# Kernel tuning notes

Measured on AMD Instinct MI355X. Metric: run time of the kernel, lower is better.

Reference implementation:

```python
import jax, jax.numpy as jnp
import numpy as np

B, S, H = 1, 2048, 2048
I = 1408            # moe intermediate size
E = 16              # n_routed_experts
K = 6               # num_experts_per_tok
G = 4               # n_group
KG = 2              # topk_group
NSH = 2             # n_shared_experts -> shared intermediate = NSH*I
RSF = 2.5           # routed_scaling_factor
CAP = 2 * (B * S * K) // E


def setup_inputs() -> dict:
    key = jax.random.key(0)
    ks = jax.random.split(key, 9)
    sh = NSH * I
    s_h = 1.0 / np.sqrt(H).astype(np.float32)
    s_i = 1.0 / np.sqrt(I).astype(np.float32)
    s_s = 1.0 / np.sqrt(sh).astype(np.float32)
    return {
        "x": jax.random.normal(ks[0], (B, S, H), jnp.float32),
        "gate_w": jax.random.normal(ks[1], (E, H), jnp.float32) * s_h,
        "gate_bias": jnp.zeros((E,), jnp.float32),
        "w_gate": jax.random.normal(ks[2], (E, H, I), jnp.float32) * s_h,
        "w_up": jax.random.normal(ks[3], (E, H, I), jnp.float32) * s_h,
        "w_down": jax.random.normal(ks[4], (E, I, H), jnp.float32) * s_i,
        "ws_gate": jax.random.normal(ks[5], (H, sh), jnp.float32) * s_h,
        "ws_up": jax.random.normal(ks[6], (H, sh), jnp.float32) * s_h,
        "ws_down": jax.random.normal(ks[7], (sh, H), jnp.float32) * s_s,
    }


def _gate(x2d, gate_w, gate_bias):
    # MoEGate: fp32 linear -> sigmoid -> noaux_tc group-limited top-k
    logits = x2d.astype(jnp.float32) @ gate_w.astype(jnp.float32).T     # [T,E]
    scores = jax.nn.sigmoid(logits)
    scores_c = scores + gate_bias                                       # e_score_correction_bias
    T = scores.shape[0]
    gs = scores_c.reshape(T, G, E // G)
    top2, _ = jax.lax.top_k(gs, 2)
    group_scores = top2.sum(-1)                                         # [T,G] sum of top-2 per group
    _, gidx = jax.lax.top_k(group_scores, KG)                           # keep top KG groups
    gmask = jnp.zeros((T, G), scores.dtype).at[jnp.arange(T)[:, None], gidx].set(1.0)
    smask = jnp.repeat(gmask, E // G, axis=1)                           # [T,E]
    tmp = jnp.where(smask > 0, scores_c, 0.0)
    _, topk_idx = jax.lax.top_k(tmp, K)                                 # [T,K]
    topk_w = jnp.take_along_axis(scores, topk_idx, axis=1)              # weights from UNbiased scores
    topk_w = topk_w / (topk_w.sum(-1, keepdims=True) + 1e-20)           # norm_topk_prob
    topk_w = topk_w * RSF
    return topk_idx, topk_w


def reference(x, gate_w, gate_bias, w_gate, w_up, w_down, ws_gate, ws_up, ws_down):
    T = B * S
    x2d = x.reshape(T, H)
    topk_idx, topk_w = _gate(x2d, gate_w, gate_bias)

    # ---- dispatch: sort (token,k) assignments by expert id (grouped-GEMM layout) ----
    flat_e = topk_idx.reshape(-1)                       # [T*K]
    order = jnp.argsort(flat_e, stable=True)
    sorted_e = flat_e[order]
    counts = jnp.bincount(flat_e, length=E)             # batch_sizes per expert
    starts = jnp.concatenate([jnp.zeros((1,), counts.dtype), jnp.cumsum(counts)[:-1]])
    pos = jnp.arange(T * K) - starts[sorted_e]          # slot within expert bucket
    tok = order // K                                    # source token of each assignment
    buf = jnp.zeros((E, CAP, H), x.dtype).at[sorted_e, pos].set(x2d[tok], mode="drop")

    # ---- grouped SwiGLU expert FFN (gmm equivalent) ----
    g = jnp.einsum("ech,ehi->eci", buf, w_gate)
    u = jnp.einsum("ech,ehi->eci", buf, w_up)
    y_e = jnp.einsum("eci,eih->ech", jax.nn.silu(g) * u, w_down)

    # ---- combine: gather back, weight, scatter-add per token ----
    keep = (pos < CAP).astype(x.dtype)
    y_sorted = y_e[sorted_e, jnp.minimum(pos, CAP - 1)] * keep[:, None]
    w_flat = topk_w.reshape(-1)[order]
    y = jnp.zeros((T, H), x.dtype).at[tok].add(y_sorted * w_flat[:, None])

    # ---- shared experts (dense SwiGLU on all tokens) ----
    sg = x2d @ ws_gate
    su = x2d @ ws_up
    y = y + (jax.nn.silu(sg) * su) @ ws_down
    return y.reshape(B, S, H)
```

## Files before the change

### kernel.cpp

```cpp
#include <hip/hip_runtime.h>

typedef unsigned short u16;
typedef u16  u16x8 __attribute__((ext_vector_type(8)));
typedef u16  u16x4 __attribute__((ext_vector_type(4)));
typedef short s16x8 __attribute__((ext_vector_type(8)));
typedef float f32x4 __attribute__((ext_vector_type(4)));

static constexpr int TT   = 2048;
static constexpr int HD   = 2048;
static constexpr int ID   = 1408;
static constexpr int NE   = 16;
static constexpr int TOPK = 6;
static constexpr int CAPE = 1536;
static constexpr int SHD  = 2816;
static constexpr float RSF_ = 2.5f;
static constexpr int PGRID = 1024;

__device__ __forceinline__ u16 f2b(float f) {
  unsigned int u = __builtin_bit_cast(unsigned int, f);
  unsigned int r = (u + 0x7FFFu + ((u >> 16) & 1u)) >> 16;
  return (u16)r;
}
__device__ __forceinline__ float b2f(u16 u) {
  unsigned int v = ((unsigned int)u) << 16;
  return __builtin_bit_cast(float, v);
}

__device__ __forceinline__ void gl_lds16(const u16* gp, u16* lp) {
  __builtin_amdgcn_global_load_lds(
      (const __attribute__((address_space(1))) void*)(unsigned long long)(const void*)gp,
      (__attribute__((address_space(3))) void*)(unsigned int)(unsigned long long)(void*)lp,
      16, 0, 0);
}

__device__ __forceinline__ void seq_map(int idx, int mtiles, int ntiles,
                                        int& bx, int& by, int& e) {
  bx = idx % mtiles;
  int tq = idx / mtiles;
  by = tq % ntiles;
  e  = tq / ntiles;
}

__global__ __launch_bounds__(256) void k_cvt(const float* __restrict__ in, u16* __restrict__ out) {
  size_t i = (size_t)blockIdx.x * 256 + threadIdx.x;
  const float4* p = (const float4*)in;
  float4 v0 = p[i * 2], v1 = p[i * 2 + 1];
  u16x8 o = { f2b(v0.x), f2b(v0.y), f2b(v0.z), f2b(v0.w),
              f2b(v1.x), f2b(v1.y), f2b(v1.z), f2b(v1.w) };
  *(u16x8*)(out + i * 8) = o;
}

__global__ __launch_bounds__(64) void k_init(int* c) {
  if (threadIdx.x < 16) c[threadIdx.x] = 0;
}

__global__ __launch_bounds__(256) void k_gate2(const float* __restrict__ x,
    const float* __restrict__ gw, const float* __restrict__ gb,
    int* __restrict__ topk_idx, float* __restrict__ topk_w) {
  const int t = threadIdx.x;
  const int tok0 = blockIdx.x * 8;
  const int i  = t >> 5;
  const int sub = t & 31;
  const int e  = sub & 15;
  const int kh = sub >> 4;
  const float4* xr = (const float4*)(x + (size_t)(tok0 + i) * HD) + kh * (HD / 8);
  const float4* wr = (const float4*)(gw + (size_t)e * HD) + kh * (HD / 8);
  float acc = 0.f;
  #pragma unroll 8
  for (int k = 0; k < HD / 8; ++k) {
    float4 a = xr[k], b = wr[k];
    acc += a.x * b.x + a.y * b.y;
    acc += a.z * b.z + a.w * b.w;
  }
  acc += __shfl_down(acc, 16);
  __shared__ float lg[8][16];
  if (sub < 16) lg[i][e] = acc;
  __syncthreads();
  if (t >= 8) return;
  const int tok = tok0 + t;
  float s[NE], sc[NE];
  #pragma unroll
  for (int ee = 0; ee < NE; ++ee) {
    s[ee]  = 1.f / (1.f + expf(-lg[t][ee]));
    sc[ee] = s[ee] + gb[ee];
  }
  float gs[4];
  #pragma unroll
  for (int g = 0; g < 4; ++g) {
    float m1 = -1e30f, m2 = -1e30f;
    #pragma unroll
    for (int j = 0; j < 4; ++j) {
      float v = sc[g * 4 + j];
      if (v > m1) { m2 = m1; m1 = v; } else if (v > m2) m2 = v;
    }
    gs[g] = m1 + m2;
  }
  int g0 = 0;
  #pragma unroll
  for (int g = 1; g < 4; ++g) if (gs[g] > gs[g0]) g0 = g;
  int g1 = -1; float g1v = -1e30f;
  #pragma unroll
  for (int g = 0; g < 4; ++g) {
    if (g == g0) continue;
    if (g1 < 0 || gs[g] > g1v) { g1 = g; g1v = gs[g]; }
  }
  float tmp[NE];
  #pragma unroll
  for (int ee = 0; ee < NE; ++ee) {
    int g = ee >> 2;
    tmp[ee] = (g == g0 || g == g1) ? sc[ee] : 0.0f;
  }
  unsigned used = 0;
  float wsum = 0.f;
  int idxs[TOPK]; float wv[TOPK];
  #pragma unroll
  for (int k = 0; k < TOPK; ++k) {
    int best = -1; float bv = -2e30f;
    #pragma unroll
    for (int ee = 0; ee < NE; ++ee) {
      bool ok = (((used >> ee) & 1u) == 0u) && (tmp[ee] > bv);
      if (ok) { bv = tmp[ee]; best = ee; }
    }
    used |= 1u << best;
    float sv = 0.f;
    #pragma unroll
    for (int ee = 0; ee < NE; ++ee) if (ee == best) sv = s[ee];
    idxs[k] = best; wv[k] = sv; wsum += sv;
  }
  float scale = RSF_ / (wsum + 1e-20f);
  #pragma unroll
  for (int k = 0; k < TOPK; ++k) {
    topk_idx[tok * TOPK + k] = idxs[k];
    topk_w[tok * TOPK + k]   = wv[k] * scale;
  }
}

__global__ __launch_bounds__(256) void k_count_pos(const int* __restrict__ topk_idx,
    int* __restrict__ rowidx, int* __restrict__ tok_of_row, int* __restrict__ counts) {
  const int e = blockIdx.x, t = threadIdx.x;
  __shared__ int pref[256];
  const int t0 = t * 8;
  int c = 0;
  for (int tt = t0; tt < t0 + 8; ++tt)
    for (int k = 0; k < TOPK; ++k) c += (topk_idx[tt * TOPK + k] == e) ? 1 : 0;
  pref[t] = c;
  __syncthreads();
  for (int off = 1; off < 256; off <<= 1) {
    int v = (t >= off) ? pref[t - off] : 0;
    __syncthreads();
    pref[t] += v;
    __syncthreads();
  }
  int run = pref[t] - c;
  if (t == 255) counts[e] = (pref[255] < CAPE) ? pref[255] : CAPE;
  for (int tt = t0; tt < t0 + 8; ++tt)
    for (int k = 0; k < TOPK; ++k)
      if (topk_idx[tt * TOPK + k] == e) {
        if (run < CAPE) {
          rowidx[tt * TOPK + k] = e * CAPE + run;
          tok_of_row[e * CAPE + run] = tt;
        } else {
          rowidx[tt * TOPK + k] = -1;
        }
        ++run;
      }
}

__global__ __launch_bounds__(256) void k_transpose_cvt(const float* __restrict__ in,
    u16* __restrict__ out, int R, int Cc, long zin, long zout) {
  __shared__ float tile[64][65];
  const float* src = in + (size_t)blockIdx.z * zin;
  u16* dst = out + (size_t)blockIdx.z * zout;
  const int r0 = blockIdx.x * 64, c0 = blockIdx.y * 64, t = threadIdx.x;
  #pragma unroll
  for (int i = 0; i < 4; ++i) {
    int c = t + 256 * i;
    int r = c >> 4, cg = (c & 15) << 2;
    float4 v = *(const float4*)(src + (size_t)(r0 + r) * Cc + c0 + cg);
    tile[r][cg + 0] = v.x; tile[r][cg + 1] = v.y;
    tile[r][cg + 2] = v.z; tile[r][cg + 3] = v.w;
  }
  __syncthreads();
  #pragma unroll
  for (int i = 0; i < 4; ++i) {
    int c = t + 256 * i;
    int oc = c >> 4, og = (c & 15) << 2;
    u16x4 w;
    #pragma unroll
    for (int j = 0; j < 4; ++j) w[j] = f2b(tile[og + j][oc]);
    *(u16x4*)(dst + (size_t)(c0 + oc) * R + r0 + og) = w;
  }
}

__global__ __launch_bounds__(256, 4) void k_pdual(
    const u16* __restrict__ A, const u16* __restrict__ B0, const u16* __restrict__ B1,
    u16* __restrict__ C, const int* __restrict__ row_map, const int* __restrict__ counts,
    int Mfixed, int K, int lda, int ldc, long b_stride, int row_cap,
    int mtiles, int ntiles, int nexp, int* __restrict__ counter) {
  const int t = threadIdx.x;
  const int l = t & 63, w = t >> 6;
  const int wm = (w >> 1) * 64, wn = (w & 1) * 32;
  const int l15 = l & 15, g0 = l >> 4;

  __shared__ __align__(16) u16 As[2][128 * 32];
  __shared__ __align__(16) u16 B0s[2][64 * 32];
  __shared__ __align__(16) u16 B1s[2][64 * 32];
  __shared__ int s_tile;

  int aoff[4], boff[2];
  #pragma unroll
  for (int i = 0; i < 4; ++i) {
    int rA = wm + i * 16 + l15;
    aoff[i] = rA * 64 + ((g0 ^ ((rA >> 1) & 3)) << 4);
  }
  #pragma unroll
  for (int i = 0; i < 2; ++i) {
    int rB = wn + i * 16 + l15;
    boff[i] = rB * 64 + ((g0 ^ ((rB >> 1) & 3)) << 4);
  }

  const int ntot = mtiles * ntiles * nexp;
  const int nk = K >> 5;
  const int cl = l15, rw = g0 * 4;

  for (;;) {
    if (t == 0) s_tile = atomicAdd(counter, 1);
    __syncthreads();
    int idx = s_tile;
    __syncthreads();
    if (idx >= ntot) break;
    int bx, by, e;
    seq_map(idx, mtiles, ntiles, bx, by, e);
    const int cnt = counts ? counts[e] : Mfixed;
    const int M_e = counts ? (cnt < row_cap ? cnt : row_cap) : Mfixed;
    const int m0 = bx * 128;
    if (m0 >= M_e) continue;
    const int n0 = by * 64;
    const int row_base = counts ? e * row_cap : 0;
    const u16* B0e = B0 + (size_t)e * b_stride;
    const u16* B1e = B1 + (size_t)e * b_stride;

    const u16 *ap[2], *b0p, *b1p;
    int loffA[2], loffB;
    #pragma unroll
    for (int i = 0; i < 2; ++i) {
      int c = t + 256 * i;
      int row = c >> 2, g = c & 3;
      int kg = g ^ ((row >> 1) & 3);
      loffA[i] = c * 8;
      int rg = m0 + row; if (rg > M_e - 1) rg = M_e - 1;
      int arow = row_map ? row_map[row_base + rg] : row_base + rg;
      ap[i] = A + (size_t)arow * lda + kg * 8;
    }
    {
      int row = t >> 2, g = t & 3;
      int kg = g ^ ((row >> 1) & 3);
      loffB = t * 8;
      b0p = B0e + (size_t)(n0 + row) * K + kg * 8;
      b1p = B1e + (size_t)(n0 + row) * K + kg * 8;
    }

    f32x4 accg[4][2], accu[4][2];
    #pragma unroll
    for (int m = 0; m < 4; ++m)
      #pragma unroll
      for (int n = 0; n < 2; ++n) { accg[m][n] = f32x4{0,0,0,0}; accu[m][n] = f32x4{0,0,0,0}; }

    #pragma unroll
    for (int i = 0; i < 2; ++i) { gl_lds16(ap[i], &As[0][loffA[i]]); ap[i] += 32; }
    gl_lds16(b0p, &B0s[0][loffB]); b0p += 32;
    gl_lds16(b1p, &B1s[0][loffB]); b1p += 32;
    __syncthreads();
    int cur = 0;
    for (int ks = 0; ks < nk; ++ks) {
      if (ks + 1 < nk) {
        #pragma unroll
        for (int i = 0; i < 2; ++i) { gl_lds16(ap[i], &As[cur ^ 1][loffA[i]]); ap[i] += 32; }
        gl_lds16(b0p, &B0s[cur ^ 1][loffB]); b0p += 32;
        gl_lds16(b1p, &B1s[cur ^ 1][loffB]); b1p += 32;
      }
      s16x8 af[4], bf0[2], bf1[2];
      #pragma unroll
      for (int i = 0; i < 4; ++i)
        af[i] = __builtin_bit_cast(s16x8, *(const u16x8*)((const char*)As[cur] + aoff[i]));
      #pragma unroll
      for (int i = 0; i < 2; ++i) {
        bf0[i] = __builtin_bit_cast(s16x8, *(const u16x8*)((const char*)B0s[cur] + boff[i]));
        bf1[i] = __builtin_bit_cast(s16x8, *(const u16x8*)((const char*)B1s[cur] + boff[i]));
      }
      #pragma unroll
      for (int m = 0; m < 4; ++m)
        #pragma unroll
        for (int n = 0; n < 2; ++n) {
          accg[m][n] = __builtin_amdgcn_mfma_f32_16x16x32_bf16(af[m], bf0[n], accg[m][n], 0, 0, 0);
          accu[m][n] = __builtin_amdgcn_mfma_f32_16x16x32_bf16(af[m], bf1[n], accu[m][n], 0, 0, 0);
        }
      __syncthreads();
      cur ^= 1;
    }

    #pragma unroll
    for (int m = 0; m < 4; ++m) {
      #pragma unroll
      for (int n = 0; n < 2; ++n) {
        f32x4 vg = accg[m][n], vu = accu[m][n];
        int gr0 = m0 + wm + m * 16 + rw;
        int gc  = n0 + wn + n * 16 + cl;
        #pragma unroll
        for (int j = 0; j < 4; ++j) {
          int rr = gr0 + j;
          if (rr < M_e) {
            float gf = vg[j];
            float act = gf / (1.f + __expf(-gf)) * vu[j];
            C[(size_t)(row_base + rr) * ldc + gc] = f2b(act);
          }
        }
      }
    }
  }
}

template <int EPI>
__global__ __launch_bounds__(256) void k_gemm3(
    const u16* __restrict__ A, const u16* __restrict__ Bt, void* __restrict__ Cptr,
    const int* __restrict__ counts, int Mfixed, int K, int lda, int ldc,
    long b_stride, int row_cap) {
  unsigned gx = gridDim.x, gy = gridDim.y, gz = gridDim.z;
  unsigned F = (blockIdx.z * gy + blockIdx.y) * gx + blockIdx.x;
  unsigned Nn = gx * gy * gz;
  unsigned q = Nn >> 3, r = Nn & 7;
  unsigned xcd = F & 7, pos = F >> 3;
  unsigned wi = (xcd < r) ? xcd * (q + 1) + pos
                          : r * (q + 1) + (xcd - r) * q + pos;
  unsigned bx = wi % gx, tq = wi / gx;
  unsigned by = tq % gy, bz = tq / gy;

  const int e = bz;
  const int cnt = counts ? counts[e] : Mfixed;
  const int M_e = counts ? (cnt < row_cap ? cnt : row_cap) : Mfixed;
  const int m0 = bx * 128;
  if (m0 >= M_e) return;
  const int n0 = by * 128;
  const int row_base = counts ? e * row_cap : 0;
  const u16* Bte = Bt + (size_t)e * b_stride;

  __shared__ __align__(16) u16 As[2][128 * 64];
  __shared__ __align__(16) u16 Bs[2][128 * 64];

  const int t = threadIdx.x;
  const int l = t & 63, w = t >> 6;
  const int wm = (w >> 1) * 64, wn = (w & 1) * 64;

  const u16 *ap[4], *bp[4];
  int loff[4];
  #pragma unroll
  for (int i = 0; i < 4; ++i) {
    int c = t + 256 * i;
    int row = c >> 3, pphys = c & 7;
    int kc = pphys ^ (row & 7);
    loff[i] = c * 8;
    int rg = m0 + row; if (rg > M_e - 1) rg = M_e - 1;
    ap[i] = A + (size_t)(row_base + rg) * lda + kc * 8;
    bp[i] = Bte + (size_t)(n0 + row) * K + kc * 8;
  }

  f32x4 acc[4][4];
  #pragma unroll
  for (int m = 0; m < 4; ++m)
    #pragma unroll
    for (int n = 0; n < 4; ++n) acc[m][n] = f32x4{0, 0, 0, 0};

  const int l15 = l & 15, g0 = l >> 4;
  int aoff[2][4], boff[2][4];
  #pragma unroll
  for (int s = 0; s < 2; ++s)
    #pragma unroll
    for (int i = 0; i < 4; ++i) {
      int rA = wm + i * 16 + l15;
      int rB = wn + i * 16 + l15;
      aoff[s][i] = rA * 128 + ((((s << 2) | g0) ^ (rA & 7)) << 4);
      boff[s][i] = rB * 128 + ((((s << 2) | g0) ^ (rB & 7)) << 4);
    }

  const int nk = K >> 6;
  #pragma unroll
  for (int i = 0; i < 4; ++i) {
    gl_lds16(ap[i], &As[0][loff[i]]); ap[i] += 64;
    gl_lds16(bp[i], &Bs[0][loff[i]]); bp[i] += 64;
  }
  __syncthreads();
  int cur = 0;
  for (int ks = 0; ks < nk; ++ks) {
    if (ks + 1 < nk) {
      #pragma unroll
      for (int i = 0; i < 4; ++i) {
        gl_lds16(ap[i], &As[cur ^ 1][loff[i]]); ap[i] += 64;
        gl_lds16(bp[i], &Bs[cur ^ 1][loff[i]]); bp[i] += 64;
      }
    }
    #pragma unroll
    for (int s = 0; s < 2; ++s) {
      s16x8 af[4], bfr[4];
      #pragma unroll
      for (int i = 0; i < 4; ++i) {
        af[i]  = __builtin_bit_cast(s16x8, *(const u16x8*)((const char*)As[cur] + aoff[s][i]));
        bfr[i] = __builtin_bit_cast(s16x8, *(const u16x8*)((const char*)Bs[cur] + boff[s][i]));
      }
      #pragma unroll
      for (int m = 0; m < 4; ++m)
        #pragma unroll
        for (int n = 0; n < 4; ++n)
          acc[m][n] = __builtin_amdgcn_mfma_f32_16x16x32_bf16(af[m], bfr[n], acc[m][n], 0, 0, 0);
    }
    __syncthreads();
    cur ^= 1;
  }

  const int cl = l15, rw = g0 * 4;
  #pragma unroll
  for (int m = 0; m < 4; ++m) {
    #pragma unroll
    for (int n = 0; n < 4; ++n) {
      f32x4 v = acc[m][n];
      int gr0 = m0 + wm + m * 16 + rw;
      int gc  = n0 + wn + n * 16 + cl;
      #pragma unroll
      for (int j = 0; j < 4; ++j) {
        int rr = gr0 + j;
        if (rr < M_e) {
          size_t ci = (size_t)(row_base + rr) * ldc + gc;
          if (EPI == 1) ((float*)Cptr)[ci] = v[j];
          else          ((u16*)Cptr)[ci]   = f2b(v[j]);
        }
      }
    }
  }
}

__global__ __launch_bounds__(256) void k_combine(const u16* __restrict__ down,
    const int* __restrict__ rowidx, const float* __restrict__ tw,
    float* __restrict__ out) {
  const int t = blockIdx.x, l = threadIdx.x;
  __shared__ int rid[TOPK];
  __shared__ float wk[TOPK];
  if (l < TOPK) { rid[l] = rowidx[t * TOPK + l]; wk[l] = tw[t * TOPK + l]; }
  __syncthreads();
  const int h0 = l * 8;
  float* op = out + (size_t)t * HD + h0;
  float4 o0 = *(float4*)op, o1 = *(float4*)(op + 4);
  float a[8] = { o0.x, o0.y, o0.z, o0.w, o1.x, o1.y, o1.z, o1.w };
  #pragma unroll
  for (int k = 0; k < TOPK; ++k) {
    int r = rid[k];
    if (r < 0) continue;
    float wkk = wk[k];
    u16x8 v = *(const u16x8*)(down + (size_t)r * HD + h0);
    #pragma unroll
    for (int j = 0; j < 8; ++j) a[j] += wkk * b2f(v[j]);
  }
  o0 = make_float4(a[0], a[1], a[2], a[3]);
  o1 = make_float4(a[4], a[5], a[6], a[7]);
  *(float4*)op = o0;
  *(float4*)(op + 4) = o1;
}

__global__ __launch_bounds__(256) void k_sentinel(float* o, int n) {
  int i = blockIdx.x * 256 + threadIdx.x;
  if (i < n) o[i] = 12345.0f;
}

extern "C" void kernel_launch(void* const* d_in, const int* in_sizes, int n_in,
                              void* d_out, int out_size, void* d_ws, size_t ws_size,
                              hipStream_t stream) {
  const float* x       = (const float*)d_in[0];
  const float* gate_w  = (const float*)d_in[1];
  const float* gate_b  = (const float*)d_in[2];
  const float* w_gate  = (const float*)d_in[3];
  const float* w_up    = (const float*)d_in[4];
  const float* w_down  = (const float*)d_in[5];
  const float* ws_gate = (const float*)d_in[6];
  const float* ws_up   = (const float*)d_in[7];
  const float* ws_down = (const float*)d_in[8];
  float* out = (float*)d_out;

  char* base = (char*)d_ws;
  char* p = base;
  auto alloc = [&](size_t bytes) -> char* {
    char* r = p;
    p += (bytes + 255) & ~(size_t)255;
    return r;
  };
  u16* slotA = (u16*)alloc((size_t)NE * ID * HD * 2);
  u16* slotB = (u16*)alloc((size_t)NE * CAPE * HD * 2);
  u16* xb    = (u16*)alloc((size_t)TT * HD * 2);
  u16* gbuf  = (u16*)alloc((size_t)NE * CAPE * ID * 2);
  u16* swTg  = (u16*)alloc((size_t)SHD * HD * 2);
  u16* swTu  = (u16*)alloc((size_t)SHD * HD * 2);
  u16* sgb   = (u16*)alloc((size_t)TT * SHD * 2);
  int*   tidx  = (int*)alloc((size_t)TT * TOPK * 4);
  float* twv   = (float*)alloc((size_t)TT * TOPK * 4);
  int*   ridx  = (int*)alloc((size_t)TT * TOPK * 4);
  int*   torow = (int*)alloc((size_t)NE * CAPE * 4);
  int*   cnts  = (int*)alloc(64);
  int*   ctrs  = (int*)alloc(64);
  u16* wTg = slotA;
  u16* wTu = slotB;
  u16* wTd = slotA;
  u16* dbuf = slotB;

  if ((size_t)(p - base) > ws_size) {
    k_sentinel<<<dim3((out_size + 255) / 256), dim3(256), 0, stream>>>(out, out_size);
    return;
  }

  dim3 b256(256);

  k_cvt<<<dim3((TT * HD) / (8 * 256)), b256, 0, stream>>>(x, xb);
  k_init<<<dim3(1), dim3(64), 0, stream>>>(ctrs);
  k_gate2<<<dim3(TT / 8), b256, 0, stream>>>(x, gate_w, gate_b, tidx, twv);
  k_count_pos<<<dim3(NE), b256, 0, stream>>>(tidx, ridx, torow, cnts);

  k_transpose_cvt<<<dim3(HD / 64, ID / 64, NE), b256, 0, stream>>>(
      w_gate, wTg, HD, ID, (long)HD * ID, (long)ID * HD);
  k_transpose_cvt<<<dim3(HD / 64, ID / 64, NE), b256, 0, stream>>>(
      w_up, wTu, HD, ID, (long)HD * ID, (long)ID * HD);
  k_pdual<<<dim3(PGRID), b256, 0, stream>>>(
      xb, wTg, wTu, gbuf, torow, cnts, 0, HD, HD, ID, (long)ID * HD, CAPE,
      CAPE / 128, ID / 64, NE, ctrs + 0);
  k_transpose_cvt<<<dim3(ID / 64, HD / 64, NE), b256, 0, stream>>>(
      w_down, wTd, ID, HD, (long)ID * HD, (long)HD * ID);
  k_gemm3<0><<<dim3(CAPE / 128, HD / 128, NE), b256, 0, stream>>>(
      gbuf, wTd, dbuf, cnts, 0, ID, ID, HD, (long)HD * ID, CAPE);

  k_transpose_cvt<<<dim3(HD / 64, SHD / 64, 1), b256, 0, stream>>>(ws_gate, swTg, HD, SHD, 0, 0);
  k_transpose_cvt<<<dim3(HD / 64, SHD / 64, 1), b256, 0, stream>>>(ws_up, swTu, HD, SHD, 0, 0);
  k_pdual<<<dim3(PGRID), b256, 0, stream>>>(
      xb, swTg, swTu, sgb, nullptr, nullptr, TT, HD, HD, SHD, 0, 0,
      TT / 128, SHD / 64, 1, ctrs + 1);
  k_transpose_cvt<<<dim3(SHD / 64, HD / 64, 1), b256, 0, stream>>>(ws_down, swTg, SHD, HD, 0, 0);
  k_gemm3<1><<<dim3(TT / 128, HD / 128, 1), b256, 0, stream>>>(
      sgb, swTg, out, nullptr, TT, SHD, SHD, HD, 0, 0);

  k_combine<<<dim3(TT), b256, 0, stream>>>(dbuf, ridx, twv, out);
}
```

Baseline: 723.5 us.

## Fold weight transpose-convert jobs into persistent dual-GEMM kernel tails

```diff
diff --git a/kernel.cpp b/kernel.cpp
--- a/kernel.cpp
+++ b/kernel.cpp
@@ -16,6 +16,14 @@
 static constexpr float RSF_ = 2.5f;
 static constexpr int PGRID = 1024;
 
+struct TJob {
+  const float* src;
+  u16* dst;
+  int R, C;
+  long zin, zout;
+  int nch;
+};
+
 __device__ __forceinline__ u16 f2b(float f) {
   unsigned int u = __builtin_bit_cast(unsigned int, f);
   unsigned int r = (u + 0x7FFFu + ((u >> 16) & 1u)) >> 16;
@@ -39,6 +47,49 @@
   int tq = idx / mtiles;
   by = tq % ntiles;
   e  = tq / ntiles;
+}
+
+__device__ __forceinline__ void run_tjobs(const TJob& j1, const TJob& j2,
+                                          int* counter2, char* pool, int& s_sh) {
+  const int t = threadIdx.x;
+  float* tile = (float*)pool;
+  const int tot = j1.nch + j2.nch;
+  for (;;) {
+    if (t == 0) s_sh = atomicAdd(counter2, 1);
+    __syncthreads();
+    int c = s_sh;
+    __syncthreads();
+    if (c >= tot) break;
+    const TJob& j = (c < j1.nch) ? j1 : j2;
+    if (c >= j1.nch) c -= j1.nch;
+    const int rt = j.R >> 6;
+    int bx = c % rt;
+    int tmp = c / rt;
+    int by = tmp % (j.C >> 6);
+    int bz = tmp / (j.C >> 6);
+    const float* src = j.src + (size_t)bz * j.zin;
+    u16* dst = j.dst + (size_t)bz * j.zout;
+    const int r0 = bx * 64, c0 = by * 64;
+    #pragma unroll
+    for (int i = 0; i < 4; ++i) {
+      int cc = t + 256 * i;
+      int r = cc >> 4, cg = (cc & 15) << 2;
+      float4 v = *(const float4*)(src + (size_t)(r0 + r) * j.C + c0 + cg);
+      tile[r * 65 + cg + 0] = v.x; tile[r * 65 + cg + 1] = v.y;
+      tile[r * 65 + cg + 2] = v.z; tile[r * 65 + cg + 3] = v.w;
+    }
+    __syncthreads();
+    #pragma unroll
+    for (int i = 0; i < 4; ++i) {
+      int cc = t + 256 * i;
+      int oc = cc >> 4, og = (cc & 15) << 2;
+      u16x4 wv;
+      #pragma unroll
+      for (int jj = 0; jj < 4; ++jj) wv[jj] = f2b(tile[(og + jj) * 65 + oc]);
+      *(u16x4*)(dst + (size_t)(c0 + oc) * j.R + r0 + og) = wv;
+    }
+    __syncthreads();
+  }
 }
 
 __global__ __launch_bounds__(256) void k_cvt(const float* __restrict__ in, u16* __restrict__ out) {
@@ -196,16 +247,18 @@
     const u16* __restrict__ A, const u16* __restrict__ B0, const u16* __restrict__ B1,
     u16* __restrict__ C, const int* __restrict__ row_map, const int* __restrict__ counts,
     int Mfixed, int K, int lda, int ldc, long b_stride, int row_cap,
-    int mtiles, int ntiles, int nexp, int* __restrict__ counter) {
+    int mtiles, int ntiles, int nexp, int* __restrict__ counter,
+    TJob j1, TJob j2, int* __restrict__ counter2) {
   const int t = threadIdx.x;
   const int l = t & 63, w = t >> 6;
   const int wm = (w >> 1) * 64, wn = (w & 1) * 32;
   const int l15 = l & 15, g0 = l >> 4;
 
-  __shared__ __align__(16) u16 As[2][128 * 32];
-  __shared__ __align__(16) u16 B0s[2][64 * 32];
-  __shared__ __align__(16) u16 B1s[2][64 * 32];
+  __shared__ __align__(16) char pool[33280];
   __shared__ int s_tile;
+  u16* Asb = (u16*)pool;
+  u16* B0b = (u16*)(pool + 16384);
+  u16* B1b = (u16*)(pool + 24576);
 
   int aoff[4], boff[2];
   #pragma unroll
@@ -267,26 +320,30 @@
       for (int n = 0; n < 2; ++n) { accg[m][n] = f32x4{0,0,0,0}; accu[m][n] = f32x4{0,0,0,0}; }
 
     #pragma unroll
-    for (int i = 0; i < 2; ++i) { gl_lds16(ap[i], &As[0][loffA[i]]); ap[i] += 32; }
-    gl_lds16(b0p, &B0s[0][loffB]); b0p += 32;
-    gl_lds16(b1p, &B1s[0][loffB]); b1p += 32;
+    for (int i = 0; i < 2; ++i) { gl_lds16(ap[i], Asb + loffA[i]); ap[i] += 32; }
+    gl_lds16(b0p, B0b + loffB); b0p += 32;
+    gl_lds16(b1p, B1b + loffB); b1p += 32;
     __syncthreads();
     int cur = 0;
     for (int ks = 0; ks < nk; ++ks) {
       if (ks + 1 < nk) {
+        int nx = cur ^ 1;
         #pragma unroll
-        for (int i = 0; i < 2; ++i) { gl_lds16(ap[i], &As[cur ^ 1][loffA[i]]); ap[i] += 32; }
-        gl_lds16(b0p, &B0s[cur ^ 1][loffB]); b0p += 32;
-        gl_lds16(b1p, &B1s[cur ^ 1][loffB]); b1p += 32;
+        for (int i = 0; i < 2; ++i) { gl_lds16(ap[i], Asb + nx * 4096 + loffA[i]); ap[i] += 32; }
+        gl_lds16(b0p, B0b + nx * 2048 + loffB); b0p += 32;
+        gl_lds16(b1p, B1b + nx * 2048 + loffB); b1p += 32;
       }
+      const char* Ab  = (const char*)Asb + cur * 8192;
+      const char* Bb0 = (const char*)B0b + cur * 4096;
+      const char* Bb1 = (const char*)B1b + cur * 4096;
       s16x8 af[4], bf0[2], bf1[2];
       #pragma unroll
       for (int i = 0; i < 4; ++i)
-        af[i] = __builtin_bit_cast(s16x8, *(const u16x8*)((const char*)As[cur] + aoff[i]));
+        af[i] = __builtin_bit_cast(s16x8, *(const u16x8*)(Ab + aoff[i]));
       #pragma unroll
       for (int i = 0; i < 2; ++i) {
-        bf0[i] = __builtin_bit_cast(s16x8, *(const u16x8*)((const char*)B0s[cur] + boff[i]));
-        bf1[i] = __builtin_bit_cast(s16x8, *(const u16x8*)((const char*)B1s[cur] + boff[i]));
+        bf0[i] = __builtin_bit_cast(s16x8, *(const u16x8*)(Bb0 + boff[i]));
+        bf1[i] = __builtin_bit_cast(s16x8, *(const u16x8*)(Bb1 + boff[i]));
       }
       #pragma unroll
       for (int m = 0; m < 4; ++m)
@@ -318,6 +375,8 @@
       }
     }
   }
+
+  run_tjobs(j1, j2, counter2, pool, s_tile);
 }
 
 template <int EPI>
@@ -496,6 +555,7 @@
   u16* gbuf  = (u16*)alloc((size_t)NE * CAPE * ID * 2);
   u16* swTg  = (u16*)alloc((size_t)SHD * HD * 2);
   u16* swTu  = (u16*)alloc((size_t)SHD * HD * 2);
+  u16* swTd  = (u16*)alloc((size_t)SHD * HD * 2);
   u16* sgb   = (u16*)alloc((size_t)TT * SHD * 2);
   int*   tidx  = (int*)alloc((size_t)TT * TOPK * 4);
   float* twv   = (float*)alloc((size_t)TT * TOPK * 4);
@@ -524,22 +584,24 @@
       w_gate, wTg, HD, ID, (long)HD * ID, (long)ID * HD);
   k_transpose_cvt<<<dim3(HD / 64, ID / 64, NE), b256, 0, stream>>>(
       w_up, wTu, HD, ID, (long)HD * ID, (long)ID * HD);
+
+  TJob jsg{ws_gate, swTg, HD, SHD, 0, 0, (HD / 64) * (SHD / 64)};
+  TJob jsu{ws_up,   swTu, HD, SHD, 0, 0, (HD / 64) * (SHD / 64)};
   k_pdual<<<dim3(PGRID), b256, 0, stream>>>(
       xb, wTg, wTu, gbuf, torow, cnts, 0, HD, HD, ID, (long)ID * HD, CAPE,
-      CAPE / 128, ID / 64, NE, ctrs + 0);
-  k_transpose_cvt<<<dim3(ID / 64, HD / 64, NE), b256, 0, stream>>>(
-      w_down, wTd, ID, HD, (long)ID * HD, (long)HD * ID);
+      CAPE / 128, ID / 64, NE, ctrs + 0, jsg, jsu, ctrs + 1);
+
+  TJob jdn{w_down,  wTd,  ID,  HD, (long)ID * HD, (long)HD * ID,
+           (ID / 64) * (HD / 64) * NE};
+  TJob jsd{ws_down, swTd, SHD, HD, 0, 0, (SHD / 64) * (HD / 64)};
+  k_pdual<<<dim3(PGRID), b256, 0, stream>>>(
+      xb, swTg, swTu, sgb, nullptr, nullptr, TT, HD, HD, SHD, 0, 0,
+      TT / 128, SHD / 64, 1, ctrs + 2, jdn, jsd, ctrs + 3);
+
   k_gemm3<0><<<dim3(CAPE / 128, HD / 128, NE), b256, 0, stream>>>(
       gbuf, wTd, dbuf, cnts, 0, ID, ID, HD, (long)HD * ID, CAPE);
-
-  k_transpose_cvt<<<dim3(HD / 64, SHD / 64, 1), b256, 0, stream>>>(ws_gate, swTg, HD, SHD, 0, 0);
-  k_transpose_cvt<<<dim3(HD / 64, SHD / 64, 1), b256, 0, stream>>>(ws_up, swTu, HD, SHD, 0, 0);
-  k_pdual<<<dim3(PGRID), b256, 0, stream>>>(
-      xb, swTg, swTu, sgb, nullptr, nullptr, TT, HD, HD, SHD, 0, 0,
-      TT / 128, SHD / 64, 1, ctrs + 1);
-  k_transpose_cvt<<<dim3(SHD / 64, HD / 64, 1), b256, 0, stream>>>(ws_down, swTg, SHD, HD, 0, 0);
   k_gemm3<1><<<dim3(TT / 128, HD / 128, 1), b256, 0, stream>>>(
-      sgb, swTg, out, nullptr, TT, SHD, SHD, HD, 0, 0);
+      sgb, swTd, out, nullptr, TT, SHD, SHD, HD, 0, 0);
 
   k_combine<<<dim3(TT), b256, 0, stream>>>(dbuf, ridx, twv, out);
 }
```

Result: slower. 781.5 us (+8.0%).
